# Kernel tuning notes

Measured on AMD Instinct MI355X. Metric: run time of the kernel, lower is better.

The kernel has to match this reference:

```python
import jax, jax.numpy as jnp
import numpy as np
from jax.scipy.special import logsumexp

TEMPERATURE = 0.1
EPS = 1e-8  # matches torch F.cosine_similarity eps


def setup_inputs() -> dict:
    key = jax.random.key(0)
    k1, k2 = jax.random.split(key)
    N, D, NUM_CLASSES = 8192, 256, 64
    embeddings = jax.random.normal(k1, (N, D), dtype=jnp.float32)
    target = jax.random.randint(k2, (N,), 0, NUM_CLASSES, dtype=jnp.int64)
    return {"embeddings": embeddings, "target": target}


def reference(embeddings, target):
    N = target.shape[0]
    # cosine similarity: normalize rows, then a single GEMM for all pairs
    norms = jnp.linalg.norm(embeddings, axis=-1, keepdims=True)
    e = embeddings / jnp.maximum(norms, EPS)
    sim = (e @ e.T) / TEMPERATURE  # [N, N]

    pos = target[:, None] == target[None, :]  # [N, N] bool, incl. diagonal
    diag = jnp.eye(N, dtype=bool)
    neg_inf = jnp.asarray(-jnp.inf, dtype=sim.dtype)

    # denominator: negatives only (positives masked to -inf)
    lse_neg = logsumexp(jnp.where(pos, neg_inf, sim), axis=1)
    # numerator: positives excluding self (diagonal masked to -inf)
    lse_pos = logsumexp(jnp.where(pos & ~diag, sim, neg_inf), axis=1)

    loss = lse_neg - lse_pos
    return loss.sum()
```

## Files before the change

### kernel.cpp

```cpp
#include <hip/hip_runtime.h>
#include <hip/hip_bf16.h>
#include <stdint.h>
#include <math.h>

#define NROWS 8192
#define DIM   256
#define RB    256
#define BI    128
#define JSUB  64
#define NBJS  8
#define JBLK  (JSUB*NBJS)
#define NG    (NROWS/JBLK)
#define NIT   (NROWS/BI)
#define NCLS  64
#define CAP   256

typedef __attribute__((ext_vector_type(4)))  int   int4v;
typedef __attribute__((ext_vector_type(8)))  int   int8v;
typedef __attribute__((ext_vector_type(16))) float floatx16;

typedef const __attribute__((address_space(1))) uint32_t gas_u32;
typedef __attribute__((address_space(3))) uint32_t las_u32;

#define SCALE_1_16 0x7B7B7B7B
#define L2E10      14.4269504088896f
#define CA_SCALE   (L2E10 * 16.0f)
#define CB_SCALE   16.0f

#if __has_builtin(__builtin_amdgcn_exp2f)
#define EXP2(x) __builtin_amdgcn_exp2f(x)
#else
#define EXP2(x) exp2f(x)
#endif

__device__ __forceinline__ void gload_lds16(const void* g, void* l) {
    __builtin_amdgcn_global_load_lds((gas_u32*)(uintptr_t)g,
                                     (las_u32*)(uintptr_t)l, 16, 0, 0);
}

__global__ __launch_bounds__(256) void normalize_kernel(const float* __restrict__ emb,
                                                        uint32_t* __restrict__ a8,
                                                        uint32_t* __restrict__ b8,
                                                        float* __restrict__ out)
{
    if (blockIdx.x == 0 && threadIdx.x == 0) *out = 0.f;
    int row  = blockIdx.x * 4 + (threadIdx.x >> 6);
    int lane = threadIdx.x & 63;
    float4 v = ((const float4*)(emb + (size_t)row * DIM))[lane];
    float ss = v.x*v.x + v.y*v.y + v.z*v.z + v.w*v.w;
    #pragma unroll
    for (int off = 32; off > 0; off >>= 1)
        ss += __shfl_xor(ss, off, 64);
    float inv = 1.0f / fmaxf(sqrtf(ss), 1e-8f);
    float ia = CA_SCALE * inv, ib = CB_SCALE * inv;
    int ra = __builtin_amdgcn_cvt_pk_fp8_f32(v.x * ia, v.y * ia, 0, false);
    ra     = __builtin_amdgcn_cvt_pk_fp8_f32(v.z * ia, v.w * ia, ra, true);
    int rb = __builtin_amdgcn_cvt_pk_fp8_f32(v.x * ib, v.y * ib, 0, false);
    rb     = __builtin_amdgcn_cvt_pk_fp8_f32(v.z * ib, v.w * ib, rb, true);
    a8[(size_t)row * 64 + lane] = (uint32_t)ra;
    b8[(size_t)row * 64 + lane] = (uint32_t)rb;
}

template<bool DIAG>
__device__ __forceinline__ void epi(const floatx16 acc[2],
                                    int jbs, int h, int ic0, float& ts)
{
    #pragma unroll
    for (int jt = 0; jt < 2; ++jt)
        #pragma unroll
        for (int rq = 0; rq < 4; ++rq)
            #pragma unroll
            for (int r2 = 0; r2 < 4; ++r2) {
                float v = EXP2(acc[jt][rq * 4 + r2]);
                if (DIAG) {
                    const int jg_ = jbs + jt * 32 + rq * 8 + h * 4 + r2;
                    if (jg_ == ic0) v = 0.f;
                }
                ts += v;
            }
}

__global__ __launch_bounds__(256, 4) void fused_kernel(const uint8_t* __restrict__ eA,
                                                       const uint8_t* __restrict__ eB,
                                                       const int* __restrict__ tgt,
                                                       float* __restrict__ pts,
                                                       float* __restrict__ sp)
{
    __shared__ uint8_t smem[2 * JSUB * RB];

    const int tid  = threadIdx.x;
    const int wave = tid >> 6;
    const int lane = tid & 63;
    const int col  = lane & 31;
    const int h    = lane >> 5;

    if (blockIdx.x < NCLS) {
        int* idx = (int*)smem;
        int* cnt = (int*)(smem + CAP * 4);
        const int c = blockIdx.x;
        if (tid == 0) *cnt = 0;
        __syncthreads();
        int4v tv[8];
        #pragma unroll
        for (int k = 0; k < 8; ++k)
            tv[k] = *(const int4v*)(tgt + k * 1024 + tid * 4);
        #pragma unroll
        for (int k = 0; k < 8; ++k)
            #pragma unroll
            for (int r = 0; r < 4; ++r)
                if (tv[k][r] == c) {
                    int p = atomicAdd(cnt, 1);
                    if (p < CAP) idx[p] = k * 1024 + tid * 4 + r;
                }
        __syncthreads();
        const int M   = min(*cnt, CAP);
        const int Mp  = (M + 31) & ~31;
        const int nbt = Mp >> 5;

        for (int bt = wave; bt < nbt; bt += 4) {
            const int b = bt * 32 + col;
            const uint8_t* pb = eB + (size_t)idx[min(b, M - 1)] * RB + h * 32;
            int8v bfr[4];
            #pragma unroll
            for (int s = 0; s < 4; ++s)
                bfr[s] = *(const int8v*)(pb + s * 64);
            float psum = 0.f;
            for (int at = 0; at < nbt; ++at) {
                const uint8_t* pa = eA + (size_t)idx[min(at * 32 + col, M - 1)] * RB + h * 32;
                floatx16 acc = (floatx16){0.f,0.f,0.f,0.f,0.f,0.f,0.f,0.f,
                                          0.f,0.f,0.f,0.f,0.f,0.f,0.f,0.f};
                #pragma unroll
                for (int s = 0; s < 4; ++s) {
                    int8v af = *(const int8v*)(pa + s * 64);
                    acc = __builtin_amdgcn_mfma_scale_f32_32x32x64_f8f6f4(
                        af, bfr[s], acc, 0, 0, 0, SCALE_1_16, 0, SCALE_1_16);
                }
                #pragma unroll
                for (int rq = 0; rq < 4; ++rq)
                    #pragma unroll
                    for (int r2 = 0; r2 < 4; ++r2) {
                        const int a = at * 32 + rq * 8 + h * 4 + r2;
                        float v = EXP2(acc[rq * 4 + r2]);
                        psum += (a != b && a < M) ? v : 0.f;
                    }
            }
            psum += __shfl_xor(psum, 32, 64);
            if (h == 0 && b < M) sp[idx[b]] = psum;
        }
        return;
    }

    const int g  = blockIdx.x - NCLS;
    const int bi = g & (NIT - 1);
    const int jg = g >> 6;

    const uint8_t* pb = eB + (size_t)(bi * BI + wave * 32 + col) * RB + h * 32;
    int8v bfr[4];
    #pragma unroll
    for (int s = 0; s < 4; ++s)
        bfr[s] = *(const int8v*)(pb + s * 64);

    int goffA[4];
    #pragma unroll
    for (int t = 0; t < 4; ++t) {
        int s   = wave * 256 + t * 64 + lane;
        int row = s >> 4;
        int lc  = (s & 15) ^ (row & 15);
        goffA[t] = row * RB + lc * 16;
    }
    const char* gA = (const char*)(eA + (size_t)jg * JBLK * RB);

    #pragma unroll
    for (int t = 0; t < 4; ++t)
        gload_lds16(gA + goffA[t], smem + wave * 4096 + t * 1024);

    const int ic0 = bi * BI + wave * 32 + col;

    const int xm = col & 15;
    int poff[4];
    #pragma unroll
    for (int s = 0; s < 4; ++s)
        poff[s] = ((s * 4 + h * 2) ^ xm) << 4;

    __syncthreads();

    float ts = 0.f;
    const int dpair = bi - jg * 4;

    #pragma unroll
    for (int bjs = 0; bjs < NBJS; ++bjs) {
        if (bjs < NBJS - 1) {
            const char* gAn = gA + (size_t)(bjs + 1) * JSUB * RB;
            #pragma unroll
            for (int t = 0; t < 4; ++t)
                gload_lds16(gAn + goffA[t],
                            smem + ((bjs + 1) & 1) * (JSUB * RB) + wave * 4096 + t * 1024);
        }

        const uint8_t* ab = smem + (bjs & 1) * (JSUB * RB);
        floatx16 acc[2];
        #pragma unroll
        for (int jt = 0; jt < 2; ++jt)
            acc[jt] = (floatx16){0.f,0.f,0.f,0.f,0.f,0.f,0.f,0.f,
                                 0.f,0.f,0.f,0.f,0.f,0.f,0.f,0.f};

        #pragma unroll
        for (int s = 0; s < 4; ++s) {
            int8v af[2];
            #pragma unroll
            for (int jt = 0; jt < 2; ++jt) {
                const uint8_t* pa = ab + (size_t)(jt * 32 + col) * RB;
                int4v lo = *(const int4v*)(pa + poff[s]);
                int4v hi = *(const int4v*)(pa + (poff[s] ^ 16));
                af[jt] = __builtin_shufflevector(lo, hi, 0, 1, 2, 3, 4, 5, 6, 7);
            }
            #pragma unroll
            for (int jt = 0; jt < 2; ++jt)
                acc[jt] = __builtin_amdgcn_mfma_scale_f32_32x32x64_f8f6f4(
                    af[jt], bfr[s], acc[jt], 0, 0,
                    0, SCALE_1_16, 0, SCALE_1_16);
        }

        const int jbs = jg * JBLK + bjs * JSUB;
        if ((bjs >> 1) == dpair)
            epi<true >(acc, jbs, h, ic0, ts);
        else
            epi<false>(acc, jbs, h, ic0, ts);

        if (bjs < NBJS - 1)
            __syncthreads();
    }

    ts += __shfl_xor(ts, 32, 64);
    if (h == 0)
        pts[(size_t)jg * NROWS + ic0] = ts;
}

__global__ __launch_bounds__(256) void finalize_kernel(const float* __restrict__ pts,
                                                       const float* __restrict__ sp,
                                                       float* __restrict__ out)
{
    const int i = blockIdx.x * 256 + threadIdx.x;
    float st = 0.f;
    #pragma unroll
    for (int t = 0; t < NG; ++t)
        st += pts[(size_t)t * NROWS + i];
    const float spv = sp[i];
    const float ns  = st - spv;
    float loss = logf(ns) - logf(spv);
    #pragma unroll
    for (int off = 32; off > 0; off >>= 1)
        loss += __shfl_xor(loss, off, 64);
    __shared__ float w4[4];
    if ((threadIdx.x & 63) == 0) w4[threadIdx.x >> 6] = loss;
    __syncthreads();
    if (threadIdx.x == 0)
        atomicAdd(out, w4[0] + w4[1] + w4[2] + w4[3]);
}

extern "C" void kernel_launch(void* const* d_in, const int* in_sizes, int n_in,
                              void* d_out, int out_size, void* d_ws, size_t ws_size,
                              hipStream_t stream)
{
    (void)in_sizes; (void)n_in; (void)out_size; (void)ws_size;
    const float* emb = (const float*)d_in[0];
    const int*   tgt = (const int*)d_in[1];
    float*       out = (float*)d_out;

    uint32_t* a8  = (uint32_t*)d_ws;
    uint32_t* b8  = a8 + (size_t)NROWS * 64;
    float*    pts = (float*)(b8 + (size_t)NROWS * 64);
    float*    sp  = pts + (size_t)NG * NROWS;

    normalize_kernel<<<NROWS / 4, 256, 0, stream>>>(emb, a8, b8, out);

    fused_kernel<<<NCLS + NIT * NG, 256, 0, stream>>>(
        (const uint8_t*)a8, (const uint8_t*)b8, tgt, pts, sp);

    finalize_kernel<<<NROWS / 256, 256, 0, stream>>>(pts, sp, out);
}
```

Baseline: 83.40 us.

## Halve j sub-tile to 32 columns and double occupancy to 8 blocks/CU

Shrinks the per-iteration j sub-tile from 64 to 32 rows, so each wave does one MFMA tile per k-step instead of two. That halves the accumulator registers and the LDS double-buffer, and launch bounds now target 8 blocks per CU instead of 4. Each block covers half as many columns, so the grid doubles (more partial sums, NG doubles). The aim is more latency hiding through occupancy, at the cost of less reuse of the B fragments per block and more barrier and launch overhead.

```diff
diff --git a/kernel.cpp b/kernel.cpp
--- a/kernel.cpp
+++ b/kernel.cpp
@@ -7,7 +7,7 @@
 #define DIM   256
 #define RB    256
 #define BI    128
-#define JSUB  64
+#define JSUB  32
 #define NBJS  8
 #define JBLK  (JSUB*NBJS)
 #define NG    (NROWS/JBLK)
@@ -62,25 +62,22 @@
 }
 
 template<bool DIAG>
-__device__ __forceinline__ void epi(const floatx16 acc[2],
-                                    int jbs, int h, int ic0, float& ts)
-{
-    #pragma unroll
-    for (int jt = 0; jt < 2; ++jt)
-        #pragma unroll
-        for (int rq = 0; rq < 4; ++rq)
-            #pragma unroll
-            for (int r2 = 0; r2 < 4; ++r2) {
-                float v = EXP2(acc[jt][rq * 4 + r2]);
-                if (DIAG) {
-                    const int jg_ = jbs + jt * 32 + rq * 8 + h * 4 + r2;
-                    if (jg_ == ic0) v = 0.f;
-                }
-                ts += v;
+__device__ __forceinline__ void epi1(const floatx16& a, int jbase, int h, int ic, float& ts)
+{
+    #pragma unroll
+    for (int rq = 0; rq < 4; ++rq)
+        #pragma unroll
+        for (int r2 = 0; r2 < 4; ++r2) {
+            float v = EXP2(a[rq * 4 + r2]);
+            if (DIAG) {
+                const int jg_ = jbase + rq * 8 + h * 4 + r2;
+                if (jg_ == ic) v = 0.f;
             }
-}
-
-__global__ __launch_bounds__(256, 4) void fused_kernel(const uint8_t* __restrict__ eA,
+            ts += v;
+        }
+}
+
+__global__ __launch_bounds__(256, 8) void fused_kernel(const uint8_t* __restrict__ eA,
                                                        const uint8_t* __restrict__ eB,
                                                        const int* __restrict__ tgt,
                                                        float* __restrict__ pts,
@@ -160,10 +157,10 @@
     for (int s = 0; s < 4; ++s)
         bfr[s] = *(const int8v*)(pb + s * 64);
 
-    int goffA[4];
-    #pragma unroll
-    for (int t = 0; t < 4; ++t) {
-        int s   = wave * 256 + t * 64 + lane;
+    int goffA[2];
+    #pragma unroll
+    for (int t = 0; t < 2; ++t) {
+        int s   = wave * 128 + t * 64 + lane;
         int row = s >> 4;
         int lc  = (s & 15) ^ (row & 15);
         goffA[t] = row * RB + lc * 16;
@@ -171,8 +168,8 @@
     const char* gA = (const char*)(eA + (size_t)jg * JBLK * RB);
 
     #pragma unroll
-    for (int t = 0; t < 4; ++t)
-        gload_lds16(gA + goffA[t], smem + wave * 4096 + t * 1024);
+    for (int t = 0; t < 2; ++t)
+        gload_lds16(gA + goffA[t], smem + wave * 2048 + t * 1024);
 
     const int ic0 = bi * BI + wave * 32 + col;
 
@@ -185,47 +182,37 @@
     __syncthreads();
 
     float ts = 0.f;
-    const int dpair = bi - jg * 4;
+    const int dquad = bi - 2 * jg;
 
     #pragma unroll
     for (int bjs = 0; bjs < NBJS; ++bjs) {
         if (bjs < NBJS - 1) {
             const char* gAn = gA + (size_t)(bjs + 1) * JSUB * RB;
             #pragma unroll
-            for (int t = 0; t < 4; ++t)
+            for (int t = 0; t < 2; ++t)
                 gload_lds16(gAn + goffA[t],
-                            smem + ((bjs + 1) & 1) * (JSUB * RB) + wave * 4096 + t * 1024);
+                            smem + ((bjs + 1) & 1) * (JSUB * RB) + wave * 2048 + t * 1024);
         }
 
         const uint8_t* ab = smem + (bjs & 1) * (JSUB * RB);
-        floatx16 acc[2];
-        #pragma unroll
-        for (int jt = 0; jt < 2; ++jt)
-            acc[jt] = (floatx16){0.f,0.f,0.f,0.f,0.f,0.f,0.f,0.f,
-                                 0.f,0.f,0.f,0.f,0.f,0.f,0.f,0.f};
+        floatx16 acc = (floatx16){0.f,0.f,0.f,0.f,0.f,0.f,0.f,0.f,
+                                  0.f,0.f,0.f,0.f,0.f,0.f,0.f,0.f};
 
         #pragma unroll
         for (int s = 0; s < 4; ++s) {
-            int8v af[2];
-            #pragma unroll
-            for (int jt = 0; jt < 2; ++jt) {
-                const uint8_t* pa = ab + (size_t)(jt * 32 + col) * RB;
-                int4v lo = *(const int4v*)(pa + poff[s]);
-                int4v hi = *(const int4v*)(pa + (poff[s] ^ 16));
-                af[jt] = __builtin_shufflevector(lo, hi, 0, 1, 2, 3, 4, 5, 6, 7);
-            }
-            #pragma unroll
-            for (int jt = 0; jt < 2; ++jt)
-                acc[jt] = __builtin_amdgcn_mfma_scale_f32_32x32x64_f8f6f4(
-                    af[jt], bfr[s], acc[jt], 0, 0,
-                    0, SCALE_1_16, 0, SCALE_1_16);
+            const uint8_t* pa = ab + (size_t)col * RB;
+            int4v lo = *(const int4v*)(pa + poff[s]);
+            int4v hi = *(const int4v*)(pa + (poff[s] ^ 16));
+            int8v af = __builtin_shufflevector(lo, hi, 0, 1, 2, 3, 4, 5, 6, 7);
+            acc = __builtin_amdgcn_mfma_scale_f32_32x32x64_f8f6f4(
+                af, bfr[s], acc, 0, 0, 0, SCALE_1_16, 0, SCALE_1_16);
         }
 
         const int jbs = jg * JBLK + bjs * JSUB;
-        if ((bjs >> 1) == dpair)
-            epi<true >(acc, jbs, h, ic0, ts);
+        if ((bjs >> 2) == dquad)
+            epi1<true >(acc, jbs, h, ic0, ts);
         else
-            epi<false>(acc, jbs, h, ic0, ts);
+            epi1<false>(acc, jbs, h, ic0, ts);
 
         if (bjs < NBJS - 1)
             __syncthreads();
```

After: 136.6 us. +63.8%, slower.

## Exploit symmetry of similarity matrix with triangular tile enumeration

Applied to the files above, without the earlier changes.

Changes the tile grid to cover only the block-triangular half of the symmetric N×N similarity matrix. Off-diagonal tiles issue a second, transposed MFMA per step so that exp-sums are produced for both row sets, with the column sums reduced through shared memory and written to extra partial-sum slots. The finalize kernel then gathers those contributions. This roughly halves the GEMM and tile-load work, at the cost of doubled MFMA and exp work per upper tile, some load imbalance between tile types, extra shared memory and a larger workspace.

```diff
diff --git a/kernel.cpp b/kernel.cpp
--- a/kernel.cpp
+++ b/kernel.cpp
@@ -8,12 +8,12 @@
 #define RB    256
 #define BI    128
 #define JSUB  64
-#define NBJS  8
+#define NBJS  4
 #define JBLK  (JSUB*NBJS)
 #define NG    (NROWS/JBLK)
-#define NIT   (NROWS/BI)
 #define NCLS  64
 #define CAP   256
+#define NTILE 1056
 
 typedef __attribute__((ext_vector_type(4)))  int   int4v;
 typedef __attribute__((ext_vector_type(8)))  int   int8v;
@@ -87,6 +87,7 @@
                                                        float* __restrict__ sp)
 {
     __shared__ uint8_t smem[2 * JSUB * RB];
+    __shared__ float   cs4[4][JBLK];
 
     const int tid  = threadIdx.x;
     const int wave = tid >> 6;
@@ -150,9 +151,13 @@
         return;
     }
 
-    const int g  = blockIdx.x - NCLS;
-    const int bi = g & (NIT - 1);
-    const int jg = g >> 6;
+    const int g = blockIdx.x - NCLS;
+    int jg = (int)((sqrtf((float)(4 * g + 1)) - 1.f) * 0.5f);
+    while ((jg + 1) * (jg + 2) <= g) ++jg;
+    while (jg * (jg + 1) > g) --jg;
+    const int bi      = g - jg * (jg + 1);
+    const bool upper  = (bi < 2 * jg);
+    const int  d      = bi - 2 * jg;
 
     const uint8_t* pb = eB + (size_t)(bi * BI + wave * 32 + col) * RB + h * 32;
     int8v bfr[4];
@@ -185,7 +190,6 @@
     __syncthreads();
 
     float ts = 0.f;
-    const int dpair = bi - jg * 4;
 
     #pragma unroll
     for (int bjs = 0; bjs < NBJS; ++bjs) {
@@ -198,34 +202,49 @@
         }
 
         const uint8_t* ab = smem + (bjs & 1) * (JSUB * RB);
-        floatx16 acc[2];
-        #pragma unroll
-        for (int jt = 0; jt < 2; ++jt)
-            acc[jt] = (floatx16){0.f,0.f,0.f,0.f,0.f,0.f,0.f,0.f,
-                                 0.f,0.f,0.f,0.f,0.f,0.f,0.f,0.f};
+        floatx16 acc[2], acc2[2];
+        #pragma unroll
+        for (int jt = 0; jt < 2; ++jt) {
+            acc[jt]  = (floatx16){0.f,0.f,0.f,0.f,0.f,0.f,0.f,0.f,
+                                  0.f,0.f,0.f,0.f,0.f,0.f,0.f,0.f};
+            acc2[jt] = acc[jt];
+        }
 
         #pragma unroll
         for (int s = 0; s < 4; ++s) {
-            int8v af[2];
             #pragma unroll
             for (int jt = 0; jt < 2; ++jt) {
                 const uint8_t* pa = ab + (size_t)(jt * 32 + col) * RB;
                 int4v lo = *(const int4v*)(pa + poff[s]);
                 int4v hi = *(const int4v*)(pa + (poff[s] ^ 16));
-                af[jt] = __builtin_shufflevector(lo, hi, 0, 1, 2, 3, 4, 5, 6, 7);
+                int8v af = __builtin_shufflevector(lo, hi, 0, 1, 2, 3, 4, 5, 6, 7);
+                acc[jt] = __builtin_amdgcn_mfma_scale_f32_32x32x64_f8f6f4(
+                    af, bfr[s], acc[jt], 0, 0, 0, SCALE_1_16, 0, SCALE_1_16);
+                if (upper)
+                    acc2[jt] = __builtin_amdgcn_mfma_scale_f32_32x32x64_f8f6f4(
+                        bfr[s], af, acc2[jt], 0, 0, 0, SCALE_1_16, 0, SCALE_1_16);
             }
-            #pragma unroll
-            for (int jt = 0; jt < 2; ++jt)
-                acc[jt] = __builtin_amdgcn_mfma_scale_f32_32x32x64_f8f6f4(
-                    af[jt], bfr[s], acc[jt], 0, 0,
-                    0, SCALE_1_16, 0, SCALE_1_16);
         }
 
         const int jbs = jg * JBLK + bjs * JSUB;
-        if ((bjs >> 1) == dpair)
-            epi<true >(acc, jbs, h, ic0, ts);
-        else
+        if (upper) {
             epi<false>(acc, jbs, h, ic0, ts);
+            #pragma unroll
+            for (int jt = 0; jt < 2; ++jt) {
+                float cp = 0.f;
+                #pragma unroll
+                for (int k = 0; k < 16; ++k)
+                    cp += EXP2(acc2[jt][k]);
+                cp += __shfl_xor(cp, 32, 64);
+                if (h == 0)
+                    cs4[wave][bjs * JSUB + jt * 32 + col] = cp;
+            }
+        } else {
+            if ((bjs >> 1) == d)
+                epi<true >(acc, jbs, h, ic0, ts);
+            else
+                epi<false>(acc, jbs, h, ic0, ts);
+        }
 
         if (bjs < NBJS - 1)
             __syncthreads();
@@ -234,17 +253,25 @@
     ts += __shfl_xor(ts, 32, 64);
     if (h == 0)
         pts[(size_t)jg * NROWS + ic0] = ts;
+
+    if (upper) {
+        __syncthreads();
+        float c = cs4[0][tid] + cs4[1][tid] + cs4[2][tid] + cs4[3][tid];
+        pts[(size_t)(NG + bi) * NROWS + jg * JBLK + tid] = c;
+    }
 }
 
 __global__ __launch_bounds__(256) void finalize_kernel(const float* __restrict__ pts,
                                                        const float* __restrict__ sp,
                                                        float* __restrict__ out)
 {
-    const int i = blockIdx.x * 256 + threadIdx.x;
+    const int jgr = blockIdx.x;
+    const int i   = blockIdx.x * 256 + threadIdx.x;
     float st = 0.f;
-    #pragma unroll
-    for (int t = 0; t < NG; ++t)
+    for (int t = jgr; t < NG; ++t)
         st += pts[(size_t)t * NROWS + i];
+    for (int b = 0; b < 2 * jgr; ++b)
+        st += pts[(size_t)(NG + b) * NROWS + i];
     const float spv = sp[i];
     const float ns  = st - spv;
     float loss = logf(ns) - logf(spv);
@@ -270,11 +297,11 @@
     uint32_t* a8  = (uint32_t*)d_ws;
     uint32_t* b8  = a8 + (size_t)NROWS * 64;
     float*    pts = (float*)(b8 + (size_t)NROWS * 64);
-    float*    sp  = pts + (size_t)NG * NROWS;
+    float*    sp  = pts + (size_t)(NG + 64) * NROWS;
 
     normalize_kernel<<<NROWS / 4, 256, 0, stream>>>(emb, a8, b8, out);
 
-    fused_kernel<<<NCLS + NIT * NG, 256, 0, stream>>>(
+    fused_kernel<<<NCLS + NTILE, 256, 0, stream>>>(
         (const uint8_t*)a8, (const uint8_t*)b8, tgt, pts, sp);
 
     finalize_kernel<<<NROWS / 256, 256, 0, stream>>>(pts, sp, out);
```

Measured after the change: 107.8 us. 1.29x slower.
